# Kernel optimization log

Hardware: AMD Instinct MI355X
Metric: run time of the kernel (lower is better)

The kernel has to match this reference:

```python
import jax, jax.numpy as jnp
import numpy as np

N_NODES = 100000
N_EDGES = 800000
NODE_F = 32
EDGE_F = 16
HID = 128
EPS = 1e-5


def _bn(h, g, b):
    # BatchNorm1d in training mode: biased batch stats over dim 0
    m = h.mean(axis=0)
    v = jnp.mean((h - m) ** 2, axis=0)
    return (h - m) * jax.lax.rsqrt(v + EPS) * g + b


def _sage(x, src, dst, Wl, bl, Wr):
    # PyG SAGEConv (mean aggr): lin_l(mean_{j->i} x_j) + lin_r(x_i)
    s = jax.ops.segment_sum(x[src], dst, num_segments=N_NODES)
    cnt = jax.ops.segment_sum(jnp.ones((src.shape[0], 1), x.dtype), dst, num_segments=N_NODES)
    mean = s / jnp.maximum(cnt, 1.0)
    return mean @ Wl + bl + x @ Wr


def setup_inputs() -> dict:
    key = jax.random.key(0)
    ks = jax.random.split(key, 32)

    def lin(k, fi, fo):
        return jax.random.normal(k, (fi, fo), jnp.float32) / np.sqrt(fi)

    inp = {
        'x': jax.random.normal(ks[0], (N_NODES, NODE_F), jnp.float32),
        'edge_index': jax.random.randint(ks[1], (2, N_EDGES), 0, N_NODES),
        'edge_attr': jax.random.normal(ks[2], (N_EDGES, EDGE_F), jnp.float32),
        'edge_source': jax.random.randint(ks[3], (N_EDGES,), 0, N_NODES),
        'edge_target': jax.random.randint(ks[4], (N_EDGES,), 0, N_NODES),
        'W1l': lin(ks[5], NODE_F, HID), 'b1': jnp.zeros((HID,), jnp.float32), 'W1r': lin(ks[6], NODE_F, HID),
        'W2l': lin(ks[7], HID, HID), 'b2': jnp.zeros((HID,), jnp.float32), 'W2r': lin(ks[8], HID, HID),
        'bn1_g': jnp.ones((HID,), jnp.float32), 'bn1_b': jnp.zeros((HID,), jnp.float32),
        'bn2_g': jnp.ones((HID,), jnp.float32), 'bn2_b': jnp.zeros((HID,), jnp.float32),
        'We': lin(ks[9], EDGE_F, HID), 'be': jnp.zeros((HID,), jnp.float32),
        'bne_g': jnp.ones((HID,), jnp.float32), 'bne_b': jnp.zeros((HID,), jnp.float32),
        'Wm1': lin(ks[10], 3 * HID, HID), 'bm1': jnp.zeros((HID,), jnp.float32),
        'bnm_g': jnp.ones((HID,), jnp.float32), 'bnm_b': jnp.zeros((HID,), jnp.float32),
        'Wm2': lin(ks[11], HID, HID // 2), 'bm2': jnp.zeros((HID // 2,), jnp.float32),
        'Wm3': lin(ks[12], HID // 2, 1), 'bm3': jnp.zeros((1,), jnp.float32),
    }
    return inp


def reference(x, edge_index, edge_attr, edge_source, edge_target,
              W1l, b1, W1r, W2l, b2, W2r, bn1_g, bn1_b, bn2_g, bn2_b,
              We, be, bne_g, bne_b, Wm1, bm1, bnm_g, bnm_b, Wm2, bm2, Wm3, bm3):
    src, dst = edge_index[0], edge_index[1]
    h = jax.nn.relu(_bn(_sage(x, src, dst, W1l, b1, W1r), bn1_g, bn1_b))  # dropout = identity (eval)
    h = jax.nn.relu(_bn(_sage(h, src, dst, W2l, b2, W2r), bn2_g, bn2_b))
    ef = _bn(jax.nn.relu(edge_attr @ We + be), bne_g, bne_b)  # Linear->ReLU->BN->Dropout(id)
    z = jnp.concatenate([h[edge_source], h[edge_target], ef], axis=1)  # [E, 3*HID]
    z = _bn(jax.nn.relu(z @ Wm1 + bm1), bnm_g, bnm_b)
    z = jax.nn.relu(z @ Wm2 + bm2)
    return (z @ Wm3 + bm3).squeeze(-1)
```

## Files before the change

kernel.cpp:

```cpp
#include <hip/hip_runtime.h>
#include <hip/hip_bf16.h>

#define NN 100000
#define NE 800000
#define SCAN_NB 98

typedef __attribute__((ext_vector_type(8))) short bf16x8;
typedef __attribute__((ext_vector_type(4))) float f32x4;

__device__ __forceinline__ short f2b(float f) {
    unsigned u = __float_as_uint(f);
    unsigned r = (u + 0x7fffu + ((u >> 16) & 1u)) >> 16;
    return (short)r;
}
__device__ __forceinline__ float b2f(short s) {
    return __uint_as_float(((unsigned)(unsigned short)s) << 16);
}

__global__ __launch_bounds__(256) void k_hist(const int* __restrict__ ei, int* __restrict__ deg)
{
    int e = blockIdx.x * 256 + threadIdx.x;
    if (e < NE) atomicAdd(&deg[ei[NE + e]], 1);
}

__global__ __launch_bounds__(1024) void k_scan_a(const int* __restrict__ deg,
    int* __restrict__ tmp, int* __restrict__ bsum)
{
    __shared__ int sh[1024];
    int t = threadIdx.x, b = blockIdx.x;
    int idx = b * 1024 + t;
    int v = (idx < NN) ? deg[idx] : 0;
    sh[t] = v;
    __syncthreads();
    for (int ofs = 1; ofs < 1024; ofs <<= 1) {
        int u = (t >= ofs) ? sh[t - ofs] : 0;
        __syncthreads();
        sh[t] += u;
        __syncthreads();
    }
    if (idx < NN) tmp[idx] = sh[t] - v;
    if (t == 1023) bsum[b] = sh[1023];
}

__global__ void k_scan_b(const int* __restrict__ bsum, int* __restrict__ boff,
    int* __restrict__ rowptr)
{
    if (threadIdx.x == 0) {
        int acc = 0;
        for (int i = 0; i < SCAN_NB; i++) { boff[i] = acc; acc += bsum[i]; }
        rowptr[NN] = acc;
    }
}

__global__ __launch_bounds__(1024) void k_scan_c(const int* __restrict__ tmp,
    const int* __restrict__ boff, int* __restrict__ rowptr, int* __restrict__ wp)
{
    int b = blockIdx.x, t = threadIdx.x;
    int idx = b * 1024 + t;
    if (idx < NN) {
        int v = boff[b] + tmp[idx];
        rowptr[idx] = v; wp[idx] = v;
    }
}

__global__ __launch_bounds__(256) void k_scatter(const int* __restrict__ ei,
    int* __restrict__ wp, int* __restrict__ elist)
{
    int e = blockIdx.x * 256 + threadIdx.x;
    if (e < NE) {
        int d = ei[NE + e];
        int pos = atomicAdd(&wp[d], 1);
        elist[pos] = ei[e];
    }
}

__global__ __launch_bounds__(256) void k_gagg1(const float* __restrict__ x,
    const int* __restrict__ rowptr, const int* __restrict__ elist, float* __restrict__ meanX)
{
    int n = blockIdx.x * 8 + (threadIdx.x >> 5);
    int j = threadIdx.x & 31;
    int b = rowptr[n], e = rowptr[n + 1];
    float acc = 0.f;
    int i = b;
    for (; i + 4 <= e; i += 4) {
        int s0 = elist[i], s1 = elist[i + 1], s2 = elist[i + 2], s3 = elist[i + 3];
        float a0 = x[(size_t)s0 * 32 + j];
        float a1 = x[(size_t)s1 * 32 + j];
        float a2 = x[(size_t)s2 * 32 + j];
        float a3 = x[(size_t)s3 * 32 + j];
        acc += (a0 + a1) + (a2 + a3);
    }
    for (; i < e; i++) acc += x[(size_t)elist[i] * 32 + j];
    float inv = (e > b) ? 1.0f / (float)(e - b) : 1.0f;
    meanX[(size_t)n * 32 + j] = acc * inv;
}

__global__ __launch_bounds__(256) void k_gagg2(const short* __restrict__ h1b,
    const int* __restrict__ rowptr, const int* __restrict__ elist,
    const float* __restrict__ sc1, const float* __restrict__ sh1, short* __restrict__ m2b)
{
    int n = blockIdx.x * 8 + (threadIdx.x >> 5);
    int c0 = (threadIdx.x & 31) * 4;
    float sc[4], sh[4];
    #pragma unroll
    for (int i = 0; i < 4; i++) { sc[i] = sc1[c0 + i]; sh[i] = sh1[c0 + i]; }
    int b = rowptr[n], e = rowptr[n + 1];
    float acc[4] = {0.f, 0.f, 0.f, 0.f};
    int i = b;
    for (; i + 4 <= e; i += 4) {
        int s0 = elist[i], s1 = elist[i + 1], s2 = elist[i + 2], s3 = elist[i + 3];
        ushort4 u0 = *(const ushort4*)(h1b + (size_t)s0 * 128 + c0);
        ushort4 u1 = *(const ushort4*)(h1b + (size_t)s1 * 128 + c0);
        ushort4 u2 = *(const ushort4*)(h1b + (size_t)s2 * 128 + c0);
        ushort4 u3 = *(const ushort4*)(h1b + (size_t)s3 * 128 + c0);
        acc[0] += fmaxf(b2f((short)u0.x) * sc[0] + sh[0], 0.f) + fmaxf(b2f((short)u1.x) * sc[0] + sh[0], 0.f)
                + fmaxf(b2f((short)u2.x) * sc[0] + sh[0], 0.f) + fmaxf(b2f((short)u3.x) * sc[0] + sh[0], 0.f);
        acc[1] += fmaxf(b2f((short)u0.y) * sc[1] + sh[1], 0.f) + fmaxf(b2f((short)u1.y) * sc[1] + sh[1], 0.f)
                + fmaxf(b2f((short)u2.y) * sc[1] + sh[1], 0.f) + fmaxf(b2f((short)u3.y) * sc[1] + sh[1], 0.f);
        acc[2] += fmaxf(b2f((short)u0.z) * sc[2] + sh[2], 0.f) + fmaxf(b2f((short)u1.z) * sc[2] + sh[2], 0.f)
                + fmaxf(b2f((short)u2.z) * sc[2] + sh[2], 0.f) + fmaxf(b2f((short)u3.z) * sc[2] + sh[2], 0.f);
        acc[3] += fmaxf(b2f((short)u0.w) * sc[3] + sh[3], 0.f) + fmaxf(b2f((short)u1.w) * sc[3] + sh[3], 0.f)
                + fmaxf(b2f((short)u2.w) * sc[3] + sh[3], 0.f) + fmaxf(b2f((short)u3.w) * sc[3] + sh[3], 0.f);
    }
    for (; i < e; i++) {
        int s = elist[i];
        ushort4 u = *(const ushort4*)(h1b + (size_t)s * 128 + c0);
        acc[0] += fmaxf(b2f((short)u.x) * sc[0] + sh[0], 0.f);
        acc[1] += fmaxf(b2f((short)u.y) * sc[1] + sh[1], 0.f);
        acc[2] += fmaxf(b2f((short)u.z) * sc[2] + sh[2], 0.f);
        acc[3] += fmaxf(b2f((short)u.w) * sc[3] + sh[3], 0.f);
    }
    float inv = (e > b) ? 1.0f / (float)(e - b) : 1.0f;
    ushort4 o;
    o.x = (unsigned short)f2b(acc[0] * inv);
    o.y = (unsigned short)f2b(acc[1] * inv);
    o.z = (unsigned short)f2b(acc[2] * inv);
    o.w = (unsigned short)f2b(acc[3] * inv);
    *(ushort4*)(m2b + (size_t)n * 128 + c0) = o;
}

__global__ __launch_bounds__(256) void k_node_l1(
    const float* __restrict__ meanX, const float* __restrict__ x,
    const float* __restrict__ Wl, const float* __restrict__ Wr,
    const float* __restrict__ bias,
    short* __restrict__ outp, float* __restrict__ ssum, float* __restrict__ ssq)
{
    __shared__ __align__(16) float sWl[32][128];
    __shared__ __align__(16) float sWr[32][128];
    __shared__ __align__(16) float sA[32][36];
    __shared__ __align__(16) float sB[32][36];
    __shared__ float red[2][128], red2[2][128];
    int tid = threadIdx.x;
    int j = tid & 127, rg = tid >> 7;
    int r0 = blockIdx.x * 32;

    for (int f = tid * 4; f < 4096; f += 1024) {
        *(float4*)((float*)sWl + f) = *(const float4*)(Wl + f);
        *(float4*)((float*)sWr + f) = *(const float4*)(Wr + f);
    }
    {
        int r = tid >> 3, c = (tid & 7) * 4;
        *(float4*)(&sA[r][c]) = *(const float4*)(meanX + (size_t)(r0 + r) * 32 + c);
        *(float4*)(&sB[r][c]) = *(const float4*)(x + (size_t)(r0 + r) * 32 + c);
    }
    __syncthreads();

    float acc[16];
    #pragma unroll
    for (int r = 0; r < 16; r++) acc[r] = 0.0f;
    int rb = rg * 16;
    #pragma unroll
    for (int kq = 0; kq < 8; kq++) {
        int k = kq * 4;
        float wl0 = sWl[k][j], wl1 = sWl[k+1][j], wl2 = sWl[k+2][j], wl3 = sWl[k+3][j];
        float wr0 = sWr[k][j], wr1 = sWr[k+1][j], wr2 = sWr[k+2][j], wr3 = sWr[k+3][j];
        #pragma unroll
        for (int r = 0; r < 16; r++) {
            float4 a = *(float4*)(&sA[rb + r][k]);
            float4 b = *(float4*)(&sB[rb + r][k]);
            acc[r] += a.x*wl0 + a.y*wl1 + a.z*wl2 + a.w*wl3
                    + b.x*wr0 + b.y*wr1 + b.z*wr2 + b.w*wr3;
        }
    }
    float bj = bias[j];
    float s1 = 0.0f, s2 = 0.0f;
    #pragma unroll
    for (int r = 0; r < 16; r++) {
        float v = acc[r] + bj;
        outp[(size_t)(r0 + rb + r) * 128 + j] = f2b(v);
        s1 += v; s2 += v * v;
    }
    red[rg][j] = s1; red2[rg][j] = s2;
    __syncthreads();
    if (rg == 0) {
        atomicAdd(&ssum[j], red[0][j] + red[1][j]);
        atomicAdd(&ssq[j],  red2[0][j] + red2[1][j]);
    }
}

__global__ __launch_bounds__(256) void k_node_l2m(
    const short* __restrict__ m2b, const short* __restrict__ h1b,
    const float* __restrict__ sc1, const float* __restrict__ sh1,
    const short* __restrict__ W2cT, const float* __restrict__ bias,
    short* __restrict__ h2b, float* __restrict__ ssum, float* __restrict__ ssq)
{
    __shared__ __align__(16) short sK[32][264];
    __shared__ float sRed[2][128];
    __shared__ float sS[128], sH[128];
    const int tid = threadIdx.x;
    const int wave = tid >> 6, lane = tid & 63, quad = lane >> 4, ln = lane & 15;
    const int waveM = wave >> 1, waveN = wave & 1;
    const int colbase = 64 * waveN, row16 = 16 * waveM;
    if (tid < 128) { sS[tid] = sc1[tid]; sH[tid] = sh1[tid]; sRed[0][tid] = 0.f; sRed[1][tid] = 0.f; }

    bf16x8 bW[4][8];
    #pragma unroll
    for (int nt = 0; nt < 4; nt++)
        #pragma unroll
        for (int kk = 0; kk < 8; kk++)
            bW[nt][kk] = *(const bf16x8*)(W2cT + (size_t)(colbase + nt * 16 + ln) * 256 + kk * 32 + quad * 8);
    float bc[4];
    #pragma unroll
    for (int nt = 0; nt < 4; nt++) bc[nt] = bias[colbase + nt * 16 + ln];

    float s1[4] = {0,0,0,0}, s2[4] = {0,0,0,0};
    f32x4 zero = {0.f, 0.f, 0.f, 0.f};
    __syncthreads();

    for (int t = blockIdx.x; t < NN / 32; t += gridDim.x) {
        int r0 = t * 32;
        __syncthreads();
        {
            int r = tid >> 3, seg = tid & 7;
            if (seg < 4) {
                const bf16x8* src = (const bf16x8*)(m2b + (size_t)(r0 + r) * 128 + seg * 32);
                bf16x8* dst = (bf16x8*)(&sK[r][seg * 32]);
                dst[0] = src[0]; dst[1] = src[1]; dst[2] = src[2]; dst[3] = src[3];
            } else {
                int c0 = (seg - 4) * 32;
                const short* src = h1b + (size_t)(r0 + r) * 128 + c0;
                short tmp[32];
                #pragma unroll
                for (int i = 0; i < 32; i++)
                    tmp[i] = f2b(fmaxf(b2f(src[i]) * sS[c0 + i] + sH[c0 + i], 0.f));
                bf16x8* dst = (bf16x8*)(&sK[r][128 + c0]);
                dst[0] = *(bf16x8*)(tmp); dst[1] = *(bf16x8*)(tmp + 8);
                dst[2] = *(bf16x8*)(tmp + 16); dst[3] = *(bf16x8*)(tmp + 24);
            }
        }
        __syncthreads();
        f32x4 acc[4] = {zero, zero, zero, zero};
        #pragma unroll
        for (int kk = 0; kk < 8; kk++) {
            bf16x8 a = *(const bf16x8*)(&sK[row16 + ln][kk * 32 + quad * 8]);
            #pragma unroll
            for (int nt = 0; nt < 4; nt++)
                acc[nt] = __builtin_amdgcn_mfma_f32_16x16x32_bf16(a, bW[nt][kk], acc[nt], 0, 0, 0);
        }
        #pragma unroll
        for (int nt = 0; nt < 4; nt++) {
            int col = colbase + nt * 16 + ln;
            #pragma unroll
            for (int r = 0; r < 4; r++) {
                float v = acc[nt][r] + bc[nt];
                h2b[(size_t)(r0 + row16 + quad * 4 + r) * 128 + col] = f2b(v);
                s1[nt] += v; s2[nt] += v * v;
            }
        }
    }
    #pragma unroll
    for (int nt = 0; nt < 4; nt++) {
        float a1 = s1[nt], a2 = s2[nt];
        a1 += __shfl_down(a1, 32); a1 += __shfl_down(a1, 16);
        a2 += __shfl_down(a2, 32); a2 += __shfl_down(a2, 16);
        if (quad == 0) {
            atomicAdd(&sRed[0][colbase + nt * 16 + ln], a1);
            atomicAdd(&sRed[1][colbase + nt * 16 + ln], a2);
        }
    }
    __syncthreads();
    if (tid < 128) {
        atomicAdd(&ssum[tid], sRed[0][tid]);
        atomicAdd(&ssq[tid],  sRed[1][tid]);
    }
}

__global__ void k_bn_fin(const float* __restrict__ ssum, const float* __restrict__ ssq,
    const float* __restrict__ g, const float* __restrict__ b, float count,
    float* __restrict__ scale, float* __restrict__ shift)
{
    int j = threadIdx.x;
    float m = ssum[j] / count;
    float var = ssq[j] / count - m * m;
    float rs = rsqrtf(var + 1e-5f);
    float sc = g[j] * rs;
    scale[j] = sc;
    shift[j] = b[j] - m * sc;
}

__global__ void k_prep(const float* __restrict__ We, const float* __restrict__ Wm1,
                       const float* __restrict__ W2l, const float* __restrict__ W2r,
                       short* __restrict__ WteT, short* __restrict__ WmsT,
                       short* __restrict__ WmdT, short* __restrict__ W2cT)
{
    int j = threadIdx.x;
    int b = blockIdx.x;
    if (b == 0) {
        for (int k = 0; k < 32; k++)
            WteT[j * 32 + k] = (k < 16) ? f2b(We[k * 128 + j]) : (short)0;
    } else if (b == 1) {
        for (int k = 0; k < 128; k++) WmsT[j * 128 + k] = f2b(Wm1[k * 128 + j]);
    } else if (b == 2) {
        for (int k = 0; k < 128; k++) WmdT[j * 128 + k] = f2b(Wm1[(128 + k) * 128 + j]);
    } else if (b == 3) {
        for (int k = 0; k < 128; k++) W2cT[j * 256 + k] = f2b(W2l[k * 128 + j]);
    } else {
        for (int k = 0; k < 128; k++) W2cT[j * 256 + 128 + k] = f2b(W2r[k * 128 + j]);
    }
}

__global__ void k_fold_e(const float* __restrict__ ssum, const float* __restrict__ ssq,
    const float* __restrict__ g, const float* __restrict__ b,
    const float* __restrict__ Wm1, const float* __restrict__ bm1,
    short* __restrict__ W1pT, float* __restrict__ bm1p)
{
    __shared__ float sa[128], sc[128];
    int tid = threadIdx.x;
    float m = ssum[tid] / (float)NE;
    float var = ssq[tid] / (float)NE - m * m;
    float rs = rsqrtf(var + 1e-5f);
    float a = g[tid] * rs;
    sa[tid] = a; sc[tid] = b[tid] - m * a;
    __syncthreads();
    float acc = bm1[tid];
    for (int k = 0; k < 128; k++) {
        float w = Wm1[(256 + k) * 128 + tid];
        W1pT[tid * 128 + k] = f2b(sa[k] * w);
        acc += sc[k] * w;
    }
    bm1p[tid] = acc;
}

__global__ void k_fold_m(const float* __restrict__ ssum, const float* __restrict__ ssq,
    const float* __restrict__ g, const float* __restrict__ b,
    const float* __restrict__ Wm2, const float* __restrict__ bm2,
    short* __restrict__ W2pT, float* __restrict__ b2p)
{
    __shared__ float sa[128], sc[128];
    int tid = threadIdx.x;
    float m = ssum[tid] / (float)NE;
    float var = ssq[tid] / (float)NE - m * m;
    float rs = rsqrtf(var + 1e-5f);
    float a = g[tid] * rs;
    sa[tid] = a; sc[tid] = b[tid] - m * a;
    __syncthreads();
    if (tid < 64) {
        float acc = bm2[tid];
        for (int k = 0; k < 128; k++) {
            float w = Wm2[k * 64 + tid];
            W2pT[tid * 128 + k] = f2b(sa[k] * w);
            acc += sc[k] * w;
        }
        b2p[tid] = acc;
    }
}

__global__ __launch_bounds__(256) void k_proj_mfma(
    const short* __restrict__ h2b, const float* __restrict__ sc2, const float* __restrict__ sh2,
    const short* __restrict__ WT0, const short* __restrict__ WT1,
    short* __restrict__ C0, short* __restrict__ C1)
{
    __shared__ __align__(16) short sA[32][136];
    __shared__ float sS[128], sH[128];
    const int tid = threadIdx.x;
    const int wave = tid >> 6, lane = tid & 63, quad = lane >> 4, ln = lane & 15;
    const int waveM = wave >> 1, waveN = wave & 1;
    const int colbase = 64 * waveN, row16 = 16 * waveM;
    const int half = (blockIdx.x >= 512) ? 1 : 0;
    const short* WT = half ? WT1 : WT0;
    short* C = half ? C1 : C0;
    const int b0 = blockIdx.x - half * 512;
    if (tid < 128) { sS[tid] = sc2[tid]; sH[tid] = sh2[tid]; }
    bf16x8 bW[4][4];
    #pragma unroll
    for (int nt = 0; nt < 4; nt++)
        #pragma unroll
        for (int kk = 0; kk < 4; kk++)
            bW[nt][kk] = *(const bf16x8*)(WT + (colbase + nt * 16 + ln) * 128 + kk * 32 + quad * 8);
    f32x4 zero = {0.f, 0.f, 0.f, 0.f};
    __syncthreads();
    for (int t = b0; t < NN / 32; t += 512) {
        int r0 = t * 32;
        __syncthreads();
        {
            int r = tid >> 3, c0 = (tid & 7) * 16;
            const short* p = h2b + (size_t)(r0 + r) * 128 + c0;
            short tmp[16];
            #pragma unroll
            for (int i = 0; i < 16; i++)
                tmp[i] = f2b(fmaxf(b2f(p[i]) * sS[c0 + i] + sH[c0 + i], 0.f));
            *(bf16x8*)(&sA[r][c0])     = *(bf16x8*)tmp;
            *(bf16x8*)(&sA[r][c0 + 8]) = *(bf16x8*)(tmp + 8);
        }
        __syncthreads();
        f32x4 acc[4] = {zero, zero, zero, zero};
        #pragma unroll
        for (int kk = 0; kk < 4; kk++) {
            bf16x8 a = *(const bf16x8*)(&sA[row16 + ln][kk * 32 + quad * 8]);
            #pragma unroll
            for (int nt = 0; nt < 4; nt++)
                acc[nt] = __builtin_amdgcn_mfma_f32_16x16x32_bf16(a, bW[nt][kk], acc[nt], 0, 0, 0);
        }
        #pragma unroll
        for (int nt = 0; nt < 4; nt++) {
            int col = colbase + nt * 16 + ln;
            #pragma unroll
            for (int r = 0; r < 4; r++)
                C[(size_t)(r0 + row16 + quad * 4 + r) * 128 + col] = f2b(acc[nt][r]);
        }
    }
}

template<int MODE, bool STOREV = false>
__global__ __launch_bounds__(256) void k_edge_mfma(
    const float* __restrict__ ea,
    const short* __restrict__ WteT, const float* __restrict__ be,
    const short* __restrict__ W1pT, const float* __restrict__ bm1p,
    const short* __restrict__ hs, const short* __restrict__ hd,
    const int* __restrict__ esrc, const int* __restrict__ etgt,
    const short* __restrict__ W2pT, const float* __restrict__ b2p,
    const float* __restrict__ Wm3, const float* __restrict__ bm3,
    float* __restrict__ ssum, float* __restrict__ ssq,
    short* __restrict__ vbuf, float* __restrict__ outp)
{
    __shared__ __align__(16) short sT[32][136];
    __shared__ __align__(16) float sSum[32][132];
    __shared__ float sRed[2][128];
    __shared__ __align__(16) short sW2[64][136];
    __shared__ float sZ[32][69];
    __shared__ float sW3[64];

    const int tid = threadIdx.x;
    const int wave = tid >> 6, lane = tid & 63;
    const int quad = lane >> 4, ln = lane & 15;
    const int waveM = wave >> 1, waveN = wave & 1;
    const int colbase = 64 * waveN, row16 = 16 * waveM;

    if (MODE < 2) {
        if (tid < 128) { sRed[0][tid] = 0.f; sRed[1][tid] = 0.f; }
    }
    if (MODE >= 2) {
        int q = tid >> 2, kb = (tid & 3) * 32;
        const bf16x8* src = (const bf16x8*)(W2pT + q * 128 + kb);
        bf16x8* dst = (bf16x8*)(&sW2[q][kb]);
        dst[0] = src[0]; dst[1] = src[1]; dst[2] = src[2]; dst[3] = src[3];
        if (tid < 64) sW3[tid] = Wm3[tid];
    }

    bf16x8 bWe[4], bW1[4][4];
    if (MODE <= 2) {
        #pragma unroll
        for (int nt = 0; nt < 4; nt++) {
            bWe[nt] = *(const bf16x8*)(WteT + (colbase + nt * 16 + ln) * 32 + quad * 8);
            if (MODE >= 1) {
                #pragma unroll
                for (int kk = 0; kk < 4; kk++)
                    bW1[nt][kk] = *(const bf16x8*)(W1pT + (colbase + nt * 16 + ln) * 128 + kk * 32 + quad * 8);
            }
        }
    }
    float bec[4], bmc[4];
    #pragma unroll
    for (int nt = 0; nt < 4; nt++) {
        bec[nt] = (MODE <= 2) ? be[colbase + nt * 16 + ln] : 0.f;
        bmc[nt] = (MODE == 1 || MODE == 2) ? bm1p[colbase + nt * 16 + ln] : 0.f;
    }
    float b2c[2] = {0.f, 0.f};
    if (MODE >= 2) { b2c[0] = b2p[32 * waveN + ln]; b2c[1] = b2p[32 * waveN + 16 + ln]; }
    float bm3v = (MODE >= 2) ? bm3[0] : 0.f;

    const int srow = tid >> 4;
    const int scol = (tid & 15) * 8;

    float s1[4] = {0,0,0,0}, s2[4] = {0,0,0,0};
    f32x4 zero = {0.f, 0.f, 0.f, 0.f};
    __syncthreads();

    if constexpr (MODE == 1) {
        const int G = gridDim.x;
        const int NT = NE / 32;
        bf16x8 gA = {}, gB = {}, gC = {}, gD = {};
        int i1sA = 0, i1tA = 0, i1sB = 0, i1tB = 0;
        float4 fe0 = {0,0,0,0}, fe1 = {0,0,0,0};

        int t = blockIdx.x;
        if (t < NT) {
            const int e0 = t * 32;
            int s0 = esrc[e0 + srow],      q0 = etgt[e0 + srow];
            int s1i = esrc[e0 + srow + 16], q1 = etgt[e0 + srow + 16];
            gA = *(const bf16x8*)(hs + (size_t)s0 * 128 + scol);
            gB = *(const bf16x8*)(hd + (size_t)q0 * 128 + scol);
            gC = *(const bf16x8*)(hs + (size_t)s1i * 128 + scol);
            gD = *(const bf16x8*)(hd + (size_t)q1 * 128 + scol);
            int t1 = t + G;
            if (t1 < NT) {
                const int e1 = t1 * 32;
                i1sA = esrc[e1 + srow];      i1tA = etgt[e1 + srow];
                i1sB = esrc[e1 + srow + 16]; i1tB = etgt[e1 + srow + 16];
            }
            if (quad < 2) {
                const float* p = ea + (size_t)(e0 + row16 + ln) * 16 + quad * 8;
                fe0 = *(const float4*)p; fe1 = *(const float4*)(p + 4);
            }
        }

        for (; t < NT; t += G) {
            const int e0 = t * 32;

            bf16x8 aE;
            #pragma unroll
            for (int i = 0; i < 8; i++) aE[i] = 0;
            if (quad < 2) {
                aE[0]=f2b(fe0.x); aE[1]=f2b(fe0.y); aE[2]=f2b(fe0.z); aE[3]=f2b(fe0.w);
                aE[4]=f2b(fe1.x); aE[5]=f2b(fe1.y); aE[6]=f2b(fe1.z); aE[7]=f2b(fe1.w);
            }
            f32x4 tacc[4];
            #pragma unroll
            for (int nt = 0; nt < 4; nt++)
                tacc[nt] = __builtin_amdgcn_mfma_f32_16x16x32_bf16(aE, bWe[nt], zero, 0, 0, 0);

            __syncthreads();

            #pragma unroll
            for (int nt = 0; nt < 4; nt++) {
                int col = colbase + nt * 16 + ln;
                #pragma unroll
                for (int r = 0; r < 4; r++)
                    sT[row16 + quad * 4 + r][col] = f2b(fmaxf(tacc[nt][r] + bec[nt], 0.f));
            }
            {
                f32x4 a0, a1, b0, b1;
                #pragma unroll
                for (int i = 0; i < 4; i++) {
                    a0[i] = b2f(gA[i])     + b2f(gB[i]);
                    a1[i] = b2f(gA[i + 4]) + b2f(gB[i + 4]);
                    b0[i] = b2f(gC[i])     + b2f(gD[i]);
                    b1[i] = b2f(gC[i + 4]) + b2f(gD[i + 4]);
                }
                *(f32x4*)(&sSum[srow][scol])          = a0;
                *(f32x4*)(&sSum[srow][scol + 4])      = a1;
                *(f32x4*)(&sSum[srow + 16][scol])     = b0;
                *(f32x4*)(&sSum[srow + 16][scol + 4]) = b1;
            }
            {
                int t1 = t + G;
                if (t1 < NT) {
                    gA = *(const bf16x8*)(hs + (size_t)i1sA * 128 + scol);
                    gB = *(const bf16x8*)(hd + (size_t)i1tA * 128 + scol);
                    gC = *(const bf16x8*)(hs + (size_t)i1sB * 128 + scol);
                    gD = *(const bf16x8*)(hd + (size_t)i1tB * 128 + scol);
                    int t2 = t1 + G;
                    if (t2 < NT) {
                        const int e2 = t2 * 32;
                        i1sA = esrc[e2 + srow];      i1tA = etgt[e2 + srow];
                        i1sB = esrc[e2 + srow + 16]; i1tB = etgt[e2 + srow + 16];
                    }
                    if (quad < 2) {
                        const float* p = ea + (size_t)(t1 * 32 + row16 + ln) * 16 + quad * 8;
                        fe0 = *(const float4*)p; fe1 = *(const float4*)(p + 4);
                    }
                }
            }
            __syncthreads();

            f32x4 uacc[4] = {zero, zero, zero, zero};
            #pragma unroll
            for (int kk = 0; kk < 4; kk++) {
                bf16x8 aU = *(const bf16x8*)(&sT[row16 + ln][kk * 32 + quad * 8]);
                #pragma unroll
                for (int nt = 0; nt < 4; nt++)
                    uacc[nt] = __builtin_amdgcn_mfma_f32_16x16x32_bf16(aU, bW1[nt][kk], uacc[nt], 0, 0, 0);
            }
            #pragma unroll
            for (int nt = 0; nt < 4; nt++) {
                int col = colbase + nt * 16 + ln;
                #pragma unroll
                for (int r = 0; r < 4; r++) {
                    float v = uacc[nt][r] + bmc[nt] + sSum[row16 + quad * 4 + r][col];
                    v = fmaxf(v, 0.f);
                    s1[nt] += v; s2[nt] += v * v;
                    if constexpr (STOREV)
                        vbuf[(size_t)(e0 + row16 + quad * 4 + r) * 128 + col] = f2b(v);
                }
            }
        }
    } else if constexpr (MODE == 0) {
        const int G = gridDim.x;
        const int NT = NE / 32;
        float4 fe0 = {0,0,0,0}, fe1 = {0,0,0,0};
        int t = blockIdx.x;
        if (t < NT && quad < 2) {
            const float* p = ea + (size_t)(t * 32 + row16 + ln) * 16 + quad * 8;
            fe0 = *(const float4*)p; fe1 = *(const float4*)(p + 4);
        }
        for (; t < NT; t += G) {
            bf16x8 aE;
            #pragma unroll
            for (int i = 0; i < 8; i++) aE[i] = 0;
            if (quad < 2) {
                aE[0]=f2b(fe0.x); aE[1]=f2b(fe0.y); aE[2]=f2b(fe0.z); aE[3]=f2b(fe0.w);
                aE[4]=f2b(fe1.x); aE[5]=f2b(fe1.y); aE[6]=f2b(fe1.z); aE[7]=f2b(fe1.w);
            }
            int t1 = t + G;
            if (t1 < NT && quad < 2) {
                const float* p = ea + (size_t)(t1 * 32 + row16 + ln) * 16 + quad * 8;
                fe0 = *(const float4*)p; fe1 = *(const float4*)(p + 4);
            }
            f32x4 tacc[4];
            #pragma unroll
            for (int nt = 0; nt < 4; nt++)
                tacc[nt] = __builtin_amdgcn_mfma_f32_16x16x32_bf16(aE, bWe[nt], zero, 0, 0, 0);
            #pragma unroll
            for (int nt = 0; nt < 4; nt++)
                #pragma unroll
                for (int r = 0; r < 4; r++) {
                    float v = fmaxf(tacc[nt][r] + bec[nt], 0.f);
                    s1[nt] += v; s2[nt] += v * v;
                }
        }
    } else if constexpr (MODE == 3) {
        const int G = gridDim.x;
        const int NT = NE / 32;
        bf16x8 aV0 = {}, aV1 = {}, aV2 = {}, aV3 = {};
        int t = blockIdx.x;
        if (t < NT) {
            const short* p = vbuf + (size_t)(t * 32 + row16 + ln) * 128 + quad * 8;
            aV0 = *(const bf16x8*)(p);
            aV1 = *(const bf16x8*)(p + 32);
            aV2 = *(const bf16x8*)(p + 64);
            aV3 = *(const bf16x8*)(p + 96);
        }
        for (; t < NT; t += G) {
            const int e0 = t * 32;
            f32x4 vacc[2] = {zero, zero};
            #pragma unroll
            for (int n2 = 0; n2 < 2; n2++) {
                bf16x8 bV0 = *(const bf16x8*)(&sW2[32 * waveN + n2 * 16 + ln][0 * 32 + quad * 8]);
                bf16x8 bV1 = *(const bf16x8*)(&sW2[32 * waveN + n2 * 16 + ln][1 * 32 + quad * 8]);
                bf16x8 bV2 = *(const bf16x8*)(&sW2[32 * waveN + n2 * 16 + ln][2 * 32 + quad * 8]);
                bf16x8 bV3 = *(const bf16x8*)(&sW2[32 * waveN + n2 * 16 + ln][3 * 32 + quad * 8]);
                vacc[n2] = __builtin_amdgcn_mfma_f32_16x16x32_bf16(aV0, bV0, vacc[n2], 0, 0, 0);
                vacc[n2] = __builtin_amdgcn_mfma_f32_16x16x32_bf16(aV1, bV1, vacc[n2], 0, 0, 0);
                vacc[n2] = __builtin_amdgcn_mfma_f32_16x16x32_bf16(aV2, bV2, vacc[n2], 0, 0, 0);
                vacc[n2] = __builtin_amdgcn_mfma_f32_16x16x32_bf16(aV3, bV3, vacc[n2], 0, 0, 0);
            }
            {
                int t1 = t + G;
                if (t1 < NT) {
                    const short* p = vbuf + (size_t)(t1 * 32 + row16 + ln) * 128 + quad * 8;
                    aV0 = *(const bf16x8*)(p);
                    aV1 = *(const bf16x8*)(p + 32);
                    aV2 = *(const bf16x8*)(p + 64);
                    aV3 = *(const bf16x8*)(p + 96);
                }
            }
            __syncthreads();
            #pragma unroll
            for (int n2 = 0; n2 < 2; n2++) {
                int col2 = 32 * waveN + n2 * 16 + ln;
                #pragma unroll
                for (int r = 0; r < 4; r++)
                    sZ[row16 + quad * 4 + r][col2] = fmaxf(vacc[n2][r] + b2c[n2], 0.f);
            }
            __syncthreads();
            {
                int row = wave * 8 + (lane >> 3);
                int ks  = (lane & 7) * 8;
                float o = 0.f;
                #pragma unroll
                for (int k2 = 0; k2 < 8; k2++)
                    o += sZ[row][ks + k2] * sW3[ks + k2];
                o += __shfl_xor(o, 1);
                o += __shfl_xor(o, 2);
                o += __shfl_xor(o, 4);
                if ((lane & 7) == 0) outp[e0 + row] = o + bm3v;
            }
        }
    } else {
    for (int t = blockIdx.x; t < NE / 32; t += gridDim.x) {
        const int e0 = t * 32;

        int isA = esrc[e0 + srow],      itA = etgt[e0 + srow];
        int isB = esrc[e0 + srow + 16], itB = etgt[e0 + srow + 16];

        bf16x8 aE;
        #pragma unroll
        for (int i = 0; i < 8; i++) aE[i] = 0;
        if (quad < 2) {
            const float* p = ea + (size_t)(e0 + row16 + ln) * 16 + quad * 8;
            float4 f0 = *(const float4*)p, f1 = *(const float4*)(p + 4);
            aE[0]=f2b(f0.x); aE[1]=f2b(f0.y); aE[2]=f2b(f0.z); aE[3]=f2b(f0.w);
            aE[4]=f2b(f1.x); aE[5]=f2b(f1.y); aE[6]=f2b(f1.z); aE[7]=f2b(f1.w);
        }
        f32x4 tacc[4];
        #pragma unroll
        for (int nt = 0; nt < 4; nt++)
            tacc[nt] = __builtin_amdgcn_mfma_f32_16x16x32_bf16(aE, bWe[nt], zero, 0, 0, 0);

        __syncthreads();
        {
            bf16x8 gA = *(const bf16x8*)(hs + (size_t)isA * 128 + scol);
            bf16x8 gB = *(const bf16x8*)(hd + (size_t)itA * 128 + scol);
            bf16x8 gC = *(const bf16x8*)(hs + (size_t)isB * 128 + scol);
            bf16x8 gD = *(const bf16x8*)(hd + (size_t)itB * 128 + scol);
            #pragma unroll
            for (int nt = 0; nt < 4; nt++) {
                int col = colbase + nt * 16 + ln;
                #pragma unroll
                for (int r = 0; r < 4; r++)
                    sT[row16 + quad * 4 + r][col] = f2b(fmaxf(tacc[nt][r] + bec[nt], 0.f));
            }
            f32x4 a0, a1, b0, b1;
            #pragma unroll
            for (int i = 0; i < 4; i++) {
                a0[i] = b2f(gA[i])     + b2f(gB[i]);
                a1[i] = b2f(gA[i + 4]) + b2f(gB[i + 4]);
                b0[i] = b2f(gC[i])     + b2f(gD[i]);
                b1[i] = b2f(gC[i + 4]) + b2f(gD[i + 4]);
            }
            *(f32x4*)(&sSum[srow][scol])          = a0;
            *(f32x4*)(&sSum[srow][scol + 4])      = a1;
            *(f32x4*)(&sSum[srow + 16][scol])     = b0;
            *(f32x4*)(&sSum[srow + 16][scol + 4]) = b1;
        }
        __syncthreads();

        f32x4 uacc[4] = {zero, zero, zero, zero};
        #pragma unroll
        for (int kk = 0; kk < 4; kk++) {
            bf16x8 aU = *(const bf16x8*)(&sT[row16 + ln][kk * 32 + quad * 8]);
            #pragma unroll
            for (int nt = 0; nt < 4; nt++)
                uacc[nt] = __builtin_amdgcn_mfma_f32_16x16x32_bf16(aU, bW1[nt][kk], uacc[nt], 0, 0, 0);
        }

        __syncthreads();
        #pragma unroll
        for (int nt = 0; nt < 4; nt++) {
            int col = colbase + nt * 16 + ln;
            #pragma unroll
            for (int r = 0; r < 4; r++) {
                float v = uacc[nt][r] + bmc[nt] + sSum[row16 + quad * 4 + r][col];
                sT[row16 + quad * 4 + r][col] = f2b(fmaxf(v, 0.f));
            }
        }
        __syncthreads();
        f32x4 vacc[2] = {zero, zero};
        #pragma unroll
        for (int kk = 0; kk < 4; kk++) {
            bf16x8 aV = *(const bf16x8*)(&sT[row16 + ln][kk * 32 + quad * 8]);
            #pragma unroll
            for (int n2 = 0; n2 < 2; n2++) {
                bf16x8 bV = *(const bf16x8*)(&sW2[32 * waveN + n2 * 16 + ln][kk * 32 + quad * 8]);
                vacc[n2] = __builtin_amdgcn_mfma_f32_16x16x32_bf16(aV, bV, vacc[n2], 0, 0, 0);
            }
        }
        #pragma unroll
        for (int n2 = 0; n2 < 2; n2++) {
            int col2 = 32 * waveN + n2 * 16 + ln;
            #pragma unroll
            for (int r = 0; r < 4; r++)
                sZ[row16 + quad * 4 + r][col2] = fmaxf(vacc[n2][r] + b2c[n2], 0.f);
        }
        __syncthreads();
        {
            int row = wave * 8 + (lane >> 3);
            int ks  = (lane & 7) * 8;
            float o = 0.f;
            #pragma unroll
            for (int k2 = 0; k2 < 8; k2++)
                o += sZ[row][ks + k2] * sW3[ks + k2];
            o += __shfl_xor(o, 1);
            o += __shfl_xor(o, 2);
            o += __shfl_xor(o, 4);
            if ((lane & 7) == 0) outp[e0 + row] = o + bm3v;
        }
    }
    }

    if (MODE < 2) {
        #pragma unroll
        for (int nt = 0; nt < 4; nt++) {
            float a1 = s1[nt], a2 = s2[nt];
            a1 += __shfl_down(a1, 32); a1 += __shfl_down(a1, 16);
            a2 += __shfl_down(a2, 32); a2 += __shfl_down(a2, 16);
            if (quad == 0) {
                atomicAdd(&sRed[0][colbase + nt * 16 + ln], a1);
                atomicAdd(&sRed[1][colbase + nt * 16 + ln], a2);
            }
        }
        __syncthreads();
        if (tid < 128) {
            atomicAdd(&ssum[tid], sRed[0][tid]);
            atomicAdd(&ssq[tid],  sRed[1][tid]);
        }
    }
}

extern "C" void kernel_launch(void* const* d_in, const int* in_sizes, int n_in,
                              void* d_out, int out_size, void* d_ws, size_t ws_size,
                              hipStream_t stream) {
    const float* x     = (const float*)d_in[0];
    const int*   ei    = (const int*)  d_in[1];
    const float* eattr = (const float*)d_in[2];
    const int*   esrc  = (const int*)  d_in[3];
    const int*   etgt  = (const int*)  d_in[4];
    const float* W1l = (const float*)d_in[5];  const float* b1 = (const float*)d_in[6];
    const float* W1r = (const float*)d_in[7];
    const float* W2l = (const float*)d_in[8];  const float* b2 = (const float*)d_in[9];
    const float* W2r = (const float*)d_in[10];
    const float* bn1_g = (const float*)d_in[11]; const float* bn1_b = (const float*)d_in[12];
    const float* bn2_g = (const float*)d_in[13]; const float* bn2_b = (const float*)d_in[14];
    const float* We  = (const float*)d_in[15]; const float* be  = (const float*)d_in[16];
    const float* bne_g = (const float*)d_in[17]; const float* bne_b = (const float*)d_in[18];
    const float* Wm1 = (const float*)d_in[19]; const float* bm1 = (const float*)d_in[20];
    const float* bnm_g = (const float*)d_in[21]; const float* bnm_b = (const float*)d_in[22];
    const float* Wm2 = (const float*)d_in[23]; const float* bm2 = (const float*)d_in[24];
    const float* Wm3 = (const float*)d_in[25]; const float* bm3 = (const float*)d_in[26];
    float* out = (float*)d_out;

    char* base = (char*)d_ws;
    size_t o = 0;
    auto A = [&](size_t bytes) { char* p = base + o; o = (o + bytes + 255) & ~(size_t)255; return p; };
    short* hsb   = (short*)A((size_t)NN * 128 * 2);
    short* hdb   = (short*)A((size_t)NN * 128 * 2);
    int*   deg   = (int*)  A((size_t)NN * 4);
    int*   rowptr= (int*)  A((size_t)(NN + 1) * 4);
    int*   wp    = (int*)  A((size_t)NN * 4);
    int*   elist = (int*)  A((size_t)NE * 4);
    float* st    = (float*)A(1024 * 4);
    int*   bsum  = (int*)  A(SCAN_NB * 4);
    int*   boff  = (int*)  A(SCAN_NB * 4);
    float* sc1   = (float*)A(512); float* sh1 = (float*)A(512);
    float* sc2   = (float*)A(512); float* sh2 = (float*)A(512);
    float* bm1p  = (float*)A(512); float* b2p = (float*)A(256);
    short* WteT  = (short*)A(128 * 32 * 2);
    short* W1pT  = (short*)A(128 * 128 * 2);
    short* WmsT  = (short*)A(128 * 128 * 2);
    short* WmdT  = (short*)A(128 * 128 * 2);
    short* W2pT  = (short*)A(64 * 128 * 2);
    short* W2cT  = (short*)A(128 * 256 * 2);
    size_t chain = o;
    float* meanX = (float*)A((size_t)NN * 32 * 4);
    short* h1b   = (short*)A((size_t)NN * 128 * 2);
    short* m2b   = (short*)A((size_t)NN * 128 * 2);
    short* h2b   = (short*)A((size_t)NN * 128 * 2);
    int*   stmp  = (int*)meanX;
    short* vbuf  = (short*)(base + chain);
    bool storev = ws_size >= chain + (size_t)NE * 128 * 2;

    hipMemsetAsync(deg, 0, (size_t)NN * 4, stream);
    hipMemsetAsync(st, 0, 1024 * 4, stream);

    k_prep<<<5, 128, 0, stream>>>(We, Wm1, W2l, W2r, WteT, WmsT, WmdT, W2cT);
    k_hist<<<(NE + 255) / 256, 256, 0, stream>>>(ei, deg);
    k_scan_a<<<SCAN_NB, 1024, 0, stream>>>(deg, stmp, bsum);
    k_scan_b<<<1, 64, 0, stream>>>(bsum, boff, rowptr);
    k_scan_c<<<SCAN_NB, 1024, 0, stream>>>(stmp, boff, rowptr, wp);
    k_scatter<<<(NE + 255) / 256, 256, 0, stream>>>(ei, wp, elist);

    k_edge_mfma<0><<<2048, 256, 0, stream>>>(eattr, WteT, be, W1pT, bm1p, hsb, hdb,
        esrc, etgt, W2pT, b2p, Wm3, bm3, st + 512, st + 640, nullptr, out);
    k_fold_e<<<1, 128, 0, stream>>>(st + 512, st + 640, bne_g, bne_b, Wm1, bm1, W1pT, bm1p);

    k_gagg1<<<NN / 8, 256, 0, stream>>>(x, rowptr, elist, meanX);
    k_node_l1<<<NN / 32, 256, 0, stream>>>(meanX, x, W1l, W1r, b1, h1b, st + 0, st + 128);
    k_bn_fin<<<1, 128, 0, stream>>>(st + 0, st + 128, bn1_g, bn1_b, (float)NN, sc1, sh1);

    k_gagg2<<<NN / 8, 256, 0, stream>>>(h1b, rowptr, elist, sc1, sh1, m2b);
    k_node_l2m<<<512, 256, 0, stream>>>(m2b, h1b, sc1, sh1, W2cT, b2, h2b, st + 256, st + 384);
    k_bn_fin<<<1, 128, 0, stream>>>(st + 256, st + 384, bn2_g, bn2_b, (float)NN, sc2, sh2);

    k_proj_mfma<<<1024, 256, 0, stream>>>(h2b, sc2, sh2, WmsT, WmdT, hsb, hdb);

    if (storev)
        k_edge_mfma<1, true><<<1024, 256, 0, stream>>>(eattr, WteT, be, W1pT, bm1p, hsb, hdb,
            esrc, etgt, W2pT, b2p, Wm3, bm3, st + 768, st + 896, vbuf, out);
    else
        k_edge_mfma<1, false><<<1024, 256, 0, stream>>>(eattr, WteT, be, W1pT, bm1p, hsb, hdb,
            esrc, etgt, W2pT, b2p, Wm3, bm3, st + 768, st + 896, nullptr, out);
    k_fold_m<<<1, 128, 0, stream>>>(st + 768, st + 896, bnm_g, bnm_b, Wm2, bm2, W2pT, b2p);

    if (storev)
        k_edge_mfma<3><<<1536, 256, 0, stream>>>(eattr, WteT, be, W1pT, bm1p, hsb, hdb,
            esrc, etgt, W2pT, b2p, Wm3, bm3, nullptr, nullptr, vbuf, out);
    else
        k_edge_mfma<2><<<1024, 256, 0, stream>>>(eattr, WteT, be, W1pT, bm1p, hsb, hdb,
            esrc, etgt, W2pT, b2p, Wm3, bm3, nullptr, nullptr, nullptr, out);
}
```

Before: 752.3 us.

## Merge small launches: fuse prep/hist, scatter/edge-stats, fold into gagg1, inline BN finalize

```diff
diff --git a/kernel.cpp b/kernel.cpp
--- a/kernel.cpp
+++ b/kernel.cpp
@@ -17,10 +17,34 @@
     return __uint_as_float(((unsigned)(unsigned short)s) << 16);
 }
 
-__global__ __launch_bounds__(256) void k_hist(const int* __restrict__ ei, int* __restrict__ deg)
-{
-    int e = blockIdx.x * 256 + threadIdx.x;
-    if (e < NE) atomicAdd(&deg[ei[NE + e]], 1);
+__global__ __launch_bounds__(256) void k_prep_hist(
+    const float* __restrict__ We, const float* __restrict__ Wm1,
+    const float* __restrict__ W2l, const float* __restrict__ W2r,
+    short* __restrict__ WteT, short* __restrict__ WmsT,
+    short* __restrict__ WmdT, short* __restrict__ W2cT,
+    const int* __restrict__ ei, int* __restrict__ deg)
+{
+    int b = blockIdx.x;
+    int tid = threadIdx.x;
+    if (b >= 5) {
+        int e = (b - 5) * 256 + tid;
+        if (e < NE) atomicAdd(&deg[ei[NE + e]], 1);
+        return;
+    }
+    if (tid >= 128) return;
+    int j = tid;
+    if (b == 0) {
+        for (int k = 0; k < 32; k++)
+            WteT[j * 32 + k] = (k < 16) ? f2b(We[k * 128 + j]) : (short)0;
+    } else if (b == 1) {
+        for (int k = 0; k < 128; k++) WmsT[j * 128 + k] = f2b(Wm1[k * 128 + j]);
+    } else if (b == 2) {
+        for (int k = 0; k < 128; k++) WmdT[j * 128 + k] = f2b(Wm1[(128 + k) * 128 + j]);
+    } else if (b == 3) {
+        for (int k = 0; k < 128; k++) W2cT[j * 256 + k] = f2b(W2l[k * 128 + j]);
+    } else {
+        for (int k = 0; k < 128; k++) W2cT[j * 256 + 128 + k] = f2b(W2r[k * 128 + j]);
+    }
 }
 
 __global__ __launch_bounds__(1024) void k_scan_a(const int* __restrict__ deg,
@@ -63,20 +87,119 @@
     }
 }
 
-__global__ __launch_bounds__(256) void k_scatter(const int* __restrict__ ei,
-    int* __restrict__ wp, int* __restrict__ elist)
-{
-    int e = blockIdx.x * 256 + threadIdx.x;
-    if (e < NE) {
-        int d = ei[NE + e];
-        int pos = atomicAdd(&wp[d], 1);
-        elist[pos] = ei[e];
-    }
-}
-
-__global__ __launch_bounds__(256) void k_gagg1(const float* __restrict__ x,
-    const int* __restrict__ rowptr, const int* __restrict__ elist, float* __restrict__ meanX)
-{
+#define SCAT_NB 3125
+__global__ __launch_bounds__(256) void k_scat_e0(
+    const int* __restrict__ ei, int* __restrict__ wp, int* __restrict__ elist,
+    const float* __restrict__ ea, const short* __restrict__ WteT, const float* __restrict__ be,
+    float* __restrict__ ssum, float* __restrict__ ssq)
+{
+    const int tid = threadIdx.x;
+    if (blockIdx.x < SCAT_NB) {
+        int e = blockIdx.x * 256 + tid;
+        if (e < NE) {
+            int d = ei[NE + e];
+            int pos = atomicAdd(&wp[d], 1);
+            elist[pos] = ei[e];
+        }
+        return;
+    }
+    __shared__ float sRed[2][128];
+    const int wave = tid >> 6, lane = tid & 63;
+    const int quad = lane >> 4, ln = lane & 15;
+    const int waveM = wave >> 1, waveN = wave & 1;
+    const int colbase = 64 * waveN, row16 = 16 * waveM;
+    if (tid < 128) { sRed[0][tid] = 0.f; sRed[1][tid] = 0.f; }
+
+    bf16x8 bWe[4];
+    float bec[4];
+    #pragma unroll
+    for (int nt = 0; nt < 4; nt++) {
+        bWe[nt] = *(const bf16x8*)(WteT + (colbase + nt * 16 + ln) * 32 + quad * 8);
+        bec[nt] = be[colbase + nt * 16 + ln];
+    }
+    float s1[4] = {0,0,0,0}, s2[4] = {0,0,0,0};
+    f32x4 zero = {0.f, 0.f, 0.f, 0.f};
+    __syncthreads();
+
+    const int G = gridDim.x - SCAT_NB;
+    const int NT = NE / 32;
+    float4 fe0 = {0,0,0,0}, fe1 = {0,0,0,0};
+    int t = blockIdx.x - SCAT_NB;
+    if (t < NT && quad < 2) {
+        const float* p = ea + (size_t)(t * 32 + row16 + ln) * 16 + quad * 8;
+        fe0 = *(const float4*)p; fe1 = *(const float4*)(p + 4);
+    }
+    for (; t < NT; t += G) {
+        bf16x8 aE;
+        #pragma unroll
+        for (int i = 0; i < 8; i++) aE[i] = 0;
+        if (quad < 2) {
+            aE[0]=f2b(fe0.x); aE[1]=f2b(fe0.y); aE[2]=f2b(fe0.z); aE[3]=f2b(fe0.w);
+            aE[4]=f2b(fe1.x); aE[5]=f2b(fe1.y); aE[6]=f2b(fe1.z); aE[7]=f2b(fe1.w);
+        }
+        int t1 = t + G;
+        if (t1 < NT && quad < 2) {
+            const float* p = ea + (size_t)(t1 * 32 + row16 + ln) * 16 + quad * 8;
+            fe0 = *(const float4*)p; fe1 = *(const float4*)(p + 4);
+        }
+        f32x4 tacc[4];
+        #pragma unroll
+        for (int nt = 0; nt < 4; nt++)
+            tacc[nt] = __builtin_amdgcn_mfma_f32_16x16x32_bf16(aE, bWe[nt], zero, 0, 0, 0);
+        #pragma unroll
+        for (int nt = 0; nt < 4; nt++)
+            #pragma unroll
+            for (int r = 0; r < 4; r++) {
+                float v = fmaxf(tacc[nt][r] + bec[nt], 0.f);
+                s1[nt] += v; s2[nt] += v * v;
+            }
+    }
+    #pragma unroll
+    for (int nt = 0; nt < 4; nt++) {
+        float a1 = s1[nt], a2 = s2[nt];
+        a1 += __shfl_down(a1, 32); a1 += __shfl_down(a1, 16);
+        a2 += __shfl_down(a2, 32); a2 += __shfl_down(a2, 16);
+        if (quad == 0) {
+            atomicAdd(&sRed[0][colbase + nt * 16 + ln], a1);
+            atomicAdd(&sRed[1][colbase + nt * 16 + ln], a2);
+        }
+    }
+    __syncthreads();
+    if (tid < 128) {
+        atomicAdd(&ssum[tid], sRed[0][tid]);
+        atomicAdd(&ssq[tid],  sRed[1][tid]);
+    }
+}
+
+__global__ __launch_bounds__(256) void k_gagg1f(const float* __restrict__ x,
+    const int* __restrict__ rowptr, const int* __restrict__ elist, float* __restrict__ meanX,
+    const float* __restrict__ essum, const float* __restrict__ essq,
+    const float* __restrict__ bne_g, const float* __restrict__ bne_b,
+    const float* __restrict__ Wm1, const float* __restrict__ bm1,
+    short* __restrict__ W1pT, float* __restrict__ bm1p)
+{
+    if (blockIdx.x == NN / 8) {
+        __shared__ float sa[128], scc[128];
+        int tid = threadIdx.x;
+        if (tid < 128) {
+            float m = essum[tid] / (float)NE;
+            float var = essq[tid] / (float)NE - m * m;
+            float rs = rsqrtf(var + 1e-5f);
+            float a = bne_g[tid] * rs;
+            sa[tid] = a; scc[tid] = bne_b[tid] - m * a;
+        }
+        __syncthreads();
+        if (tid < 128) {
+            float acc = bm1[tid];
+            for (int k = 0; k < 128; k++) {
+                float w = Wm1[(256 + k) * 128 + tid];
+                W1pT[tid * 128 + k] = f2b(sa[k] * w);
+                acc += scc[k] * w;
+            }
+            bm1p[tid] = acc;
+        }
+        return;
+    }
     int n = blockIdx.x * 8 + (threadIdx.x >> 5);
     int j = threadIdx.x & 31;
     int b = rowptr[n], e = rowptr[n + 1];
@@ -97,13 +220,20 @@
 
 __global__ __launch_bounds__(256) void k_gagg2(const short* __restrict__ h1b,
     const int* __restrict__ rowptr, const int* __restrict__ elist,
-    const float* __restrict__ sc1, const float* __restrict__ sh1, short* __restrict__ m2b)
+    const float* __restrict__ ssum1, const float* __restrict__ ssq1,
+    const float* __restrict__ g1, const float* __restrict__ b1g, short* __restrict__ m2b)
 {
     int n = blockIdx.x * 8 + (threadIdx.x >> 5);
     int c0 = (threadIdx.x & 31) * 4;
     float sc[4], sh[4];
     #pragma unroll
-    for (int i = 0; i < 4; i++) { sc[i] = sc1[c0 + i]; sh[i] = sh1[c0 + i]; }
+    for (int i = 0; i < 4; i++) {
+        float m = ssum1[c0 + i] / (float)NN;
+        float var = ssq1[c0 + i] / (float)NN - m * m;
+        float rs = rsqrtf(var + 1e-5f);
+        float s = g1[c0 + i] * rs;
+        sc[i] = s; sh[i] = b1g[c0 + i] - m * s;
+    }
     int b = rowptr[n], e = rowptr[n + 1];
     float acc[4] = {0.f, 0.f, 0.f, 0.f};
     int i = b;
@@ -200,7 +330,8 @@
 
 __global__ __launch_bounds__(256) void k_node_l2m(
     const short* __restrict__ m2b, const short* __restrict__ h1b,
-    const float* __restrict__ sc1, const float* __restrict__ sh1,
+    const float* __restrict__ ssum1, const float* __restrict__ ssq1,
+    const float* __restrict__ g1, const float* __restrict__ b1g,
     const short* __restrict__ W2cT, const float* __restrict__ bias,
     short* __restrict__ h2b, float* __restrict__ ssum, float* __restrict__ ssq)
 {
@@ -211,7 +342,14 @@
     const int wave = tid >> 6, lane = tid & 63, quad = lane >> 4, ln = lane & 15;
     const int waveM = wave >> 1, waveN = wave & 1;
     const int colbase = 64 * waveN, row16 = 16 * waveM;
-    if (tid < 128) { sS[tid] = sc1[tid]; sH[tid] = sh1[tid]; sRed[0][tid] = 0.f; sRed[1][tid] = 0.f; }
+    if (tid < 128) {
+        float m = ssum1[tid] / (float)NN;
+        float var = ssq1[tid] / (float)NN - m * m;
+        float rs = rsqrtf(var + 1e-5f);
+        float s = g1[tid] * rs;
+        sS[tid] = s; sH[tid] = b1g[tid] - m * s;
+        sRed[0][tid] = 0.f; sRed[1][tid] = 0.f;
+    }
 
     bf16x8 bW[4][8];
     #pragma unroll
@@ -285,62 +423,6 @@
     }
 }
 
-__global__ void k_bn_fin(const float* __restrict__ ssum, const float* __restrict__ ssq,
-    const float* __restrict__ g, const float* __restrict__ b, float count,
-    float* __restrict__ scale, float* __restrict__ shift)
-{
-    int j = threadIdx.x;
-    float m = ssum[j] / count;
-    float var = ssq[j] / count - m * m;
-    float rs = rsqrtf(var + 1e-5f);
-    float sc = g[j] * rs;
-    scale[j] = sc;
-    shift[j] = b[j] - m * sc;
-}
-
-__global__ void k_prep(const float* __restrict__ We, const float* __restrict__ Wm1,
-                       const float* __restrict__ W2l, const float* __restrict__ W2r,
-                       short* __restrict__ WteT, short* __restrict__ WmsT,
-                       short* __restrict__ WmdT, short* __restrict__ W2cT)
-{
-    int j = threadIdx.x;
-    int b = blockIdx.x;
-    if (b == 0) {
-        for (int k = 0; k < 32; k++)
-            WteT[j * 32 + k] = (k < 16) ? f2b(We[k * 128 + j]) : (short)0;
-    } else if (b == 1) {
-        for (int k = 0; k < 128; k++) WmsT[j * 128 + k] = f2b(Wm1[k * 128 + j]);
-    } else if (b == 2) {
-        for (int k = 0; k < 128; k++) WmdT[j * 128 + k] = f2b(Wm1[(128 + k) * 128 + j]);
-    } else if (b == 3) {
-        for (int k = 0; k < 128; k++) W2cT[j * 256 + k] = f2b(W2l[k * 128 + j]);
-    } else {
-        for (int k = 0; k < 128; k++) W2cT[j * 256 + 128 + k] = f2b(W2r[k * 128 + j]);
-    }
-}
-
-__global__ void k_fold_e(const float* __restrict__ ssum, const float* __restrict__ ssq,
-    const float* __restrict__ g, const float* __restrict__ b,
-    const float* __restrict__ Wm1, const float* __restrict__ bm1,
-    short* __restrict__ W1pT, float* __restrict__ bm1p)
-{
-    __shared__ float sa[128], sc[128];
-    int tid = threadIdx.x;
-    float m = ssum[tid] / (float)NE;
-    float var = ssq[tid] / (float)NE - m * m;
-    float rs = rsqrtf(var + 1e-5f);
-    float a = g[tid] * rs;
-    sa[tid] = a; sc[tid] = b[tid] - m * a;
-    __syncthreads();
-    float acc = bm1[tid];
-    for (int k = 0; k < 128; k++) {
-        float w = Wm1[(256 + k) * 128 + tid];
-        W1pT[tid * 128 + k] = f2b(sa[k] * w);
-        acc += sc[k] * w;
-    }
-    bm1p[tid] = acc;
-}
-
 __global__ void k_fold_m(const float* __restrict__ ssum, const float* __restrict__ ssq,
     const float* __restrict__ g, const float* __restrict__ b,
     const float* __restrict__ Wm2, const float* __restrict__ bm2,
@@ -366,7 +448,9 @@
 }
 
 __global__ __launch_bounds__(256) void k_proj_mfma(
-    const short* __restrict__ h2b, const float* __restrict__ sc2, const float* __restrict__ sh2,
+    const short* __restrict__ h2b,
+    const float* __restrict__ ssum2, const float* __restrict__ ssq2,
+    const float* __restrict__ g2, const float* __restrict__ b2g,
     const short* __restrict__ WT0, const short* __restrict__ WT1,
     short* __restrict__ C0, short* __restrict__ C1)
 {
@@ -380,7 +464,13 @@
     const short* WT = half ? WT1 : WT0;
     short* C = half ? C1 : C0;
     const int b0 = blockIdx.x - half * 512;
-    if (tid < 128) { sS[tid] = sc2[tid]; sH[tid] = sh2[tid]; }
+    if (tid < 128) {
+        float m = ssum2[tid] / (float)NN;
+        float var = ssq2[tid] / (float)NN - m * m;
+        float rs = rsqrtf(var + 1e-5f);
+        float s = g2[tid] * rs;
+        sS[tid] = s; sH[tid] = b2g[tid] - m * s;
+    }
     bf16x8 bW[4][4];
     #pragma unroll
     for (int nt = 0; nt < 4; nt++)
@@ -436,6 +526,7 @@
     __shared__ __align__(16) short sT[32][136];
     __shared__ __align__(16) float sSum[32][132];
     __shared__ float sRed[2][128];
+    __shared__ __align__(16) short sWe[128][16];
     __shared__ __align__(16) short sW2[64][136];
     __shared__ float sZ[32][69];
     __shared__ float sW3[64];
@@ -448,6 +539,10 @@
 
     if (MODE < 2) {
         if (tid < 128) { sRed[0][tid] = 0.f; sRed[1][tid] = 0.f; }
+    }
+    if (MODE <= 2) {
+        int r = tid >> 1, cs = (tid & 1) * 8;
+        *(bf16x8*)(&sWe[r][cs]) = *(const bf16x8*)(WteT + r * 32 + cs);
     }
     if (MODE >= 2) {
         int q = tid >> 2, kb = (tid & 3) * 32;
@@ -457,17 +552,13 @@
         if (tid < 64) sW3[tid] = Wm3[tid];
     }
 
-    bf16x8 bWe[4], bW1[4][4];
-    if (MODE <= 2) {
-        #pragma unroll
-        for (int nt = 0; nt < 4; nt++) {
-            bWe[nt] = *(const bf16x8*)(WteT + (colbase + nt * 16 + ln) * 32 + quad * 8);
-            if (MODE >= 1) {
-                #pragma unroll
-                for (int kk = 0; kk < 4; kk++)
-                    bW1[nt][kk] = *(const bf16x8*)(W1pT + (colbase + nt * 16 + ln) * 128 + kk * 32 + quad * 8);
-            }
-        }
+    bf16x8 bW1[4][4];
+    if (MODE == 1 || MODE == 2) {
+        #pragma unroll
+        for (int nt = 0; nt < 4; nt++)
+            #pragma unroll
+            for (int kk = 0; kk < 4; kk++)
+                bW1[nt][kk] = *(const bf16x8*)(W1pT + (colbase + nt * 16 + ln) * 128 + kk * 32 + quad * 8);
     }
     float bec[4], bmc[4];
     #pragma unroll
@@ -526,8 +617,10 @@
             }
             f32x4 tacc[4];
             #pragma unroll
-            for (int nt = 0; nt < 4; nt++)
-                tacc[nt] = __builtin_amdgcn_mfma_f32_16x16x32_bf16(aE, bWe[nt], zero, 0, 0, 0);
+            for (int nt = 0; nt < 4; nt++) {
+                bf16x8 bWe_ = *(const bf16x8*)(&sWe[colbase + nt * 16 + ln][(quad & 1) * 8]);
+                tacc[nt] = __builtin_amdgcn_mfma_f32_16x16x32_bf16(aE, bWe_, zero, 0, 0, 0);
+            }
 
             __syncthreads();
 
@@ -594,40 +687,6 @@
                 }
             }
         }
-    } else if constexpr (MODE == 0) {
-        const int G = gridDim.x;
-        const int NT = NE / 32;
-        float4 fe0 = {0,0,0,0}, fe1 = {0,0,0,0};
-        int t = blockIdx.x;
-        if (t < NT && quad < 2) {
-            const float* p = ea + (size_t)(t * 32 + row16 + ln) * 16 + quad * 8;
-            fe0 = *(const float4*)p; fe1 = *(const float4*)(p + 4);
-        }
-        for (; t < NT; t += G) {
-            bf16x8 aE;
-            #pragma unroll
-            for (int i = 0; i < 8; i++) aE[i] = 0;
-            if (quad < 2) {
-                aE[0]=f2b(fe0.x); aE[1]=f2b(fe0.y); aE[2]=f2b(fe0.z); aE[3]=f2b(fe0.w);
-                aE[4]=f2b(fe1.x); aE[5]=f2b(fe1.y); aE[6]=f2b(fe1.z); aE[7]=f2b(fe1.w);
-            }
-            int t1 = t + G;
-            if (t1 < NT && quad < 2) {
-                const float* p = ea + (size_t)(t1 * 32 + row16 + ln) * 16 + quad * 8;
-                fe0 = *(const float4*)p; fe1 = *(const float4*)(p + 4);
-            }
-            f32x4 tacc[4];
-            #pragma unroll
-            for (int nt = 0; nt < 4; nt++)
-                tacc[nt] = __builtin_amdgcn_mfma_f32_16x16x32_bf16(aE, bWe[nt], zero, 0, 0, 0);
-            #pragma unroll
-            for (int nt = 0; nt < 4; nt++)
-                #pragma unroll
-                for (int r = 0; r < 4; r++) {
-                    float v = fmaxf(tacc[nt][r] + bec[nt], 0.f);
-                    s1[nt] += v; s2[nt] += v * v;
-                }
-        }
     } else if constexpr (MODE == 3) {
         const int G = gridDim.x;
         const int NT = NE / 32;
@@ -704,8 +763,10 @@
         }
         f32x4 tacc[4];
         #pragma unroll
-        for (int nt = 0; nt < 4; nt++)
-            tacc[nt] = __builtin_amdgcn_mfma_f32_16x16x32_bf16(aE, bWe[nt], zero, 0, 0, 0);
+        for (int nt = 0; nt < 4; nt++) {
+            bf16x8 bWe_ = *(const bf16x8*)(&sWe[colbase + nt * 16 + ln][(quad & 1) * 8]);
+            tacc[nt] = __builtin_amdgcn_mfma_f32_16x16x32_bf16(aE, bWe_, zero, 0, 0, 0);
+        }
 
         __syncthreads();
         {
@@ -862,32 +923,31 @@
     hipMemsetAsync(deg, 0, (size_t)NN * 4, stream);
     hipMemsetAsync(st, 0, 1024 * 4, stream);
 
-    k_prep<<<5, 128, 0, stream>>>(We, Wm1, W2l, W2r, WteT, WmsT, WmdT, W2cT);
-    k_hist<<<(NE + 255) / 256, 256, 0, stream>>>(ei, deg);
+    k_prep_hist<<<5 + (NE + 255) / 256, 256, 0, stream>>>(We, Wm1, W2l, W2r,
+        WteT, WmsT, WmdT, W2cT, ei, deg);
     k_scan_a<<<SCAN_NB, 1024, 0, stream>>>(deg, stmp, bsum);
     k_scan_b<<<1, 64, 0, stream>>>(bsum, boff, rowptr);
     k_scan_c<<<SCAN_NB, 1024, 0, stream>>>(stmp, boff, rowptr, wp);
-    k_scatter<<<(NE + 255) / 256, 256, 0, stream>>>(ei, wp, elist);
-
-    k_edge_mfma<0><<<2048, 256, 0, stream>>>(eattr, WteT, be, W1pT, bm1p, hsb, hdb,
-        esrc, etgt, W2pT, b2p, Wm3, bm3, st + 512, st + 640, nullptr, out);
-    k_fold_e<<<1, 128, 0, stream>>>(st + 512, st + 640, bne_g, bne_b, Wm1, bm1, W1pT, bm1p);
-
-    k_gagg1<<<NN / 8, 256, 0, stream>>>(x, rowptr, elist, meanX);
+
+    k_scat_e0<<<SCAT_NB + 2048, 256, 0, stream>>>(ei, wp, elist,
+        eattr, WteT, be, st + 512, st + 640);
+
+    k_gagg1f<<<NN / 8 + 1, 256, 0, stream>>>(x, rowptr, elist, meanX,
+        st + 512, st + 640, bne_g, bne_b, Wm1, bm1, W1pT, bm1p);
     k_node_l1<<<NN / 32, 256, 0, stream>>>(meanX, x, W1l, W1r, b1, h1b, st + 0, st + 128);
-    k_bn_fin<<<1, 128, 0, stream>>>(st + 0, st + 128, bn1_g, bn1_b, (float)NN, sc1, sh1);
-
-    k_gagg2<<<NN / 8, 256, 0, stream>>>(h1b, rowptr, elist, sc1, sh1, m2b);
-    k_node_l2m<<<512, 256, 0, stream>>>(m2b, h1b, sc1, sh1, W2cT, b2, h2b, st + 256, st + 384);
-    k_bn_fin<<<1, 128, 0, stream>>>(st + 256, st + 384, bn2_g, bn2_b, (float)NN, sc2, sh2);
-
-    k_proj_mfma<<<1024, 256, 0, stream>>>(h2b, sc2, sh2, WmsT, WmdT, hsb, hdb);
+
+    k_gagg2<<<NN / 8, 256, 0, stream>>>(h1b, rowptr, elist, st + 0, st + 128, bn1_g, bn1_b, m2b);
+    k_node_l2m<<<512, 256, 0, stream>>>(m2b, h1b, st + 0, st + 128, bn1_g, bn1_b,
+        W2cT, b2, h2b, st + 256, st + 384);
+
+    k_proj_mfma<<<1024, 256, 0, stream>>>(h2b, st + 256, st + 384, bn2_g, bn2_b,
+        WmsT, WmdT, hsb, hdb);
 
     if (storev)
-        k_edge_mfma<1, true><<<1024, 256, 0, stream>>>(eattr, WteT, be, W1pT, bm1p, hsb, hdb,
+        k_edge_mfma<1, true><<<1280, 256, 0, stream>>>(eattr, WteT, be, W1pT, bm1p, hsb, hdb,
             esrc, etgt, W2pT, b2p, Wm3, bm3, st + 768, st + 896, vbuf, out);
     else
-        k_edge_mfma<1, false><<<1024, 256, 0, stream>>>(eattr, WteT, be, W1pT, bm1p, hsb, hdb,
+        k_edge_mfma<1, false><<<1280, 256, 0, stream>>>(eattr, WteT, be, W1pT, bm1p, hsb, hdb,
             esrc, etgt, W2pT, b2p, Wm3, bm3, st + 768, st + 896, nullptr, out);
     k_fold_m<<<1, 128, 0, stream>>>(st + 768, st + 896, bnm_g, bnm_b, Wm2, bm2, W2pT, b2p);
 
```

Result: no change. 756.2 us (+0.5%).
